# Kernel tuning notes

Measured on AMD Instinct MI355X. Metric: run time of the kernel, lower is better.

The kernel has to match this reference:

```python
import jax, jax.numpy as jnp
import numpy as np

N_NODES = 50000
N_EDGES = 800000
D_FEAT = 96
HIDDEN = 96
AVG_DEG = 16.0


def setup_inputs() -> dict:
    key = jax.random.key(0)
    k1, k2, k3, k4, k5 = jax.random.split(key, 5)
    x = jax.random.normal(k1, (N_NODES, D_FEAT), dtype=jnp.float32)
    row = jax.random.randint(k2, (N_EDGES,), 0, N_NODES)
    col = jax.random.randint(k3, (N_EDGES,), 0, N_NODES)
    edge_index = jnp.stack([row, col]).astype(jnp.int32)  # [2, E]
    # normalized adjacency values ~ 1/degree scale
    edge_weight = jax.random.uniform(k4, (N_EDGES,), dtype=jnp.float32) / AVG_DEG
    # init_w: small normal + identity (random=False path)
    W = 0.1 * jax.random.normal(k5, (D_FEAT, HIDDEN), dtype=jnp.float32) + jnp.eye(D_FEAT, HIDDEN, dtype=jnp.float32)
    b = jnp.zeros((HIDDEN,), dtype=jnp.float32)
    return {"x": x, "W": W, "b": b, "edge_index": edge_index, "edge_weight": edge_weight}


def reference(x, W, b, edge_index, edge_weight):
    # dense projection + bias
    h = x @ W + b  # [N, H]
    # sparse adj matmul: out[i] = sum_e w_e * h[col_e] for row_e == i
    row, col = edge_index[0], edge_index[1]
    msgs = edge_weight[:, None] * h[col]  # [E, H]
    pre_nonlinearity = jax.ops.segment_sum(msgs, row, num_segments=N_NODES)  # [N, H]
    # inference path: no dropout (training=None)
    output = jax.nn.elu(pre_nonlinearity)
    return (pre_nonlinearity, output)
```

## Files before the change

### kernel.cpp

```cpp
#include <hip/hip_runtime.h>


#define D 96
#define BSHIFT 5
#define BROWS 32
#define CAP 768
#define NSEGB 256
#define SCAP 16
#define NBKT_MAX 1600
#define GR 64
#define NFRAG 18

typedef unsigned long long u64;
typedef unsigned short u16;
typedef unsigned int u32;

typedef __attribute__((ext_vector_type(8))) __bf16 bf8_t;
typedef __attribute__((ext_vector_type(8))) short s8_t;
typedef __attribute__((ext_vector_type(4))) float f4_t;

__device__ __forceinline__ u16 f2bf(float f) {
  const u32 u = __float_as_uint(f);
  return (u16)((u + 0x7FFFu + ((u >> 16) & 1u)) >> 16);
}
__device__ __forceinline__ float bf2f(u16 s) {
  return __uint_as_float(((u32)s) << 16);
}

__device__ __forceinline__ f4_t mfma16(s8_t a, s8_t b, f4_t c) {
  return __builtin_amdgcn_mfma_f32_16x16x32_bf16(
      __builtin_bit_cast(bf8_t, a), __builtin_bit_cast(bf8_t, b), c, 0, 0, 0);
}

__device__ __forceinline__ void acc4(const u64* __restrict__ se, int k,
                                     const u16* __restrict__ h16, int lane,
                                     float& a0, float& a1, float& a2) {
  const u64 u0 = se[k], u1 = se[k + 1], u2 = se[k + 2], u3 = se[k + 3];
  const u16* h0 = h16 + (size_t)(u0 & 0xFFFFF) * D;
  const u16* h1 = h16 + (size_t)(u1 & 0xFFFFF) * D;
  const u16* h2 = h16 + (size_t)(u2 & 0xFFFFF) * D;
  const u16* h3 = h16 + (size_t)(u3 & 0xFFFFF) * D;
  const float w0 = __uint_as_float((u32)(u0 >> 32));
  const float w1 = __uint_as_float((u32)(u1 >> 32));
  const float w2 = __uint_as_float((u32)(u2 >> 32));
  const float w3 = __uint_as_float((u32)(u3 >> 32));
  const float p00 = bf2f(h0[lane]), p01 = bf2f(h0[lane + 32]), p02 = bf2f(h0[lane + 64]);
  const float p10 = bf2f(h1[lane]), p11 = bf2f(h1[lane + 32]), p12 = bf2f(h1[lane + 64]);
  const float p20 = bf2f(h2[lane]), p21 = bf2f(h2[lane + 32]), p22 = bf2f(h2[lane + 64]);
  const float p30 = bf2f(h3[lane]), p31 = bf2f(h3[lane + 32]), p32 = bf2f(h3[lane + 64]);
  a0 = fmaf(w0, p00, a0); a1 = fmaf(w0, p01, a1); a2 = fmaf(w0, p02, a2);
  a0 = fmaf(w1, p10, a0); a1 = fmaf(w1, p11, a1); a2 = fmaf(w1, p12, a2);
  a0 = fmaf(w2, p20, a0); a1 = fmaf(w2, p21, a1); a2 = fmaf(w2, p22, a2);
  a0 = fmaf(w3, p30, a0); a1 = fmaf(w3, p31, a1); a2 = fmaf(w3, p32, a2);
}

__device__ __forceinline__ void acc1(const u64* __restrict__ se, int k,
                                     const u16* __restrict__ h16, int lane,
                                     float& a0, float& a1, float& a2) {
  const u64 u = se[k];
  const u16* hr = h16 + (size_t)(u & 0xFFFFF) * D;
  const float w = __uint_as_float((u32)(u >> 32));
  a0 = fmaf(w, bf2f(hr[lane]), a0);
  a1 = fmaf(w, bf2f(hr[lane + 32]), a1);
  a2 = fmaf(w, bf2f(hr[lane + 64]), a2);
}

__global__ __launch_bounds__(256) void setup_kernel(
    const float* __restrict__ W, u16* __restrict__ whi, u16* __restrict__ wlo) {
  const int i = blockIdx.x * 256 + threadIdx.x;
  if (i < NFRAG * 64) {
    const int f = i >> 6;
    const int lane = i & 63;
    const int n = f / 3, kt = f - 3 * n;
    const int g = lane >> 4, l15 = lane & 15;
    const int col = n * 16 + l15;
#pragma unroll
    for (int j = 0; j < 8; ++j) {
      const float w = W[(kt * 32 + 8 * g + j) * D + col];
      const u16 hb = f2bf(w);
      whi[(size_t)(f * 64 + lane) * 8 + j] = hb;
      wlo[(size_t)(f * 64 + lane) * 8 + j] = f2bf(w - bf2f(hb));
    }
  }
}

__global__ __launch_bounds__(256) void fused_gemm_bucketize(
    const float* __restrict__ x, const u16* __restrict__ whi,
    const u16* __restrict__ wlo, const float* __restrict__ bias,
    u16* __restrict__ h16, int n_nodes,
    const int* __restrict__ rows, const int* __restrict__ cols,
    const float* __restrict__ ew, int* __restrict__ cnt_g,
    u64* __restrict__ tmp2, int n_edges, int nbkt, int echunk) {
  __shared__ int cur[NBKT_MAX];
  const int tid = threadIdx.x;

  if ((int)blockIdx.x < NSEGB) {
    const int blk = blockIdx.x;
    for (int i = tid; i < NBKT_MAX; i += 256) cur[i] = 0;
    __syncthreads();
    const int e0 = blk * echunk;
    const int e1 = min(e0 + echunk, n_edges);
    for (int e = e0 + tid; e < e1; e += 256) {
      const int r = rows[e];
      const int c = cols[e];
      const float w = ew[e];
      const int b = r >> BSHIFT;
      const u64 u = ((u64)__float_as_uint(w) << 32) |
                    ((u64)(r & (BROWS - 1)) << 20) | (u64)(unsigned)c;
      const int pos = atomicAdd(&cur[b], 1);
      if (pos < SCAP) tmp2[((size_t)b * NSEGB + blk) * SCAP + pos] = u;
    }
    __syncthreads();
    for (int b = tid; b < nbkt; b += 256)
      cnt_g[(size_t)b * NSEGB + blk] = min(cur[b], SCAP);
  } else {
    const int wid = tid >> 6;
    const int lane = tid & 63;
    const int l15 = lane & 15;
    const int g = lane >> 4;
    const int row0 = ((int)blockIdx.x - NSEGB) * GR + wid * 16;

    const int ra = min(row0 + l15, n_nodes - 1);
    const float* xr = x + (size_t)ra * D;
    s8_t ah[3], al[3];
#pragma unroll
    for (int kt = 0; kt < 3; ++kt) {
      const float4 v0 = *(const float4*)(xr + kt * 32 + 8 * g);
      const float4 v1 = *(const float4*)(xr + kt * 32 + 8 * g + 4);
      const float vv[8] = {v0.x, v0.y, v0.z, v0.w, v1.x, v1.y, v1.z, v1.w};
#pragma unroll
      for (int j = 0; j < 8; ++j) {
        const u16 hb = f2bf(vv[j]);
        ah[kt][j] = (short)hb;
        al[kt][j] = (short)f2bf(vv[j] - bf2f(hb));
      }
    }

    f4_t acc[6];
#pragma unroll
    for (int n = 0; n < 6; ++n) {
      const float bv = bias[n * 16 + l15];
      acc[n][0] = bv; acc[n][1] = bv; acc[n][2] = bv; acc[n][3] = bv;
    }

#pragma unroll
    for (int kt = 0; kt < 3; ++kt) {
#pragma unroll
      for (int n = 0; n < 6; ++n) {
        const int f = n * 3 + kt;
        const s8_t bh = *(const s8_t*)(whi + (size_t)(f * 64 + lane) * 8);
        const s8_t bl = *(const s8_t*)(wlo + (size_t)(f * 64 + lane) * 8);
        acc[n] = mfma16(ah[kt], bh, acc[n]);
        acc[n] = mfma16(al[kt], bh, acc[n]);
        acc[n] = mfma16(ah[kt], bl, acc[n]);
      }
    }

#pragma unroll
    for (int n = 0; n < 6; ++n) {
#pragma unroll
      for (int r = 0; r < 4; ++r) {
        const int row = row0 + 4 * g + r;
        if (row < n_nodes)
          h16[(size_t)row * D + n * 16 + l15] = f2bf(acc[n][r]);
      }
    }
  }
}

__global__ __launch_bounds__(256) void bucket_gather_kernel(
    const int* __restrict__ cnt_g, const u64* __restrict__ tmp2,
    const u16* __restrict__ h16, float* __restrict__ pre,
    float* __restrict__ out, int n_nodes) {
  __shared__ u64 raw[CAP];
  __shared__ u64 se[CAP];
  __shared__ int segcnt[NSEGB];
  __shared__ int segoff[NSEGB + 1];
  __shared__ int wtot[4];
  __shared__ int cnt[BROWS];
  __shared__ int off[BROWS + 1];
  __shared__ int cur[BROWS];
  const int tid = threadIdx.x;
  const int b = blockIdx.x;
  if (tid < BROWS) cnt[tid] = 0;

  const int c = min(cnt_g[(size_t)b * NSEGB + tid], SCAP);
  segcnt[tid] = c;
  int incl = c;
#pragma unroll
  for (int d = 1; d < 64; d <<= 1) {
    const int v = __shfl_up(incl, d, 64);
    if ((tid & 63) >= d) incl += v;
  }
  if ((tid & 63) == 63) wtot[tid >> 6] = incl;
  __syncthreads();
  const int w = tid >> 6;
  int wbase = 0;
#pragma unroll
  for (int ww = 0; ww < 3; ++ww)
    if (ww < w) wbase += wtot[ww];
  segoff[tid + 1] = wbase + incl;
  if (tid == 0) segoff[0] = 0;
  __syncthreads();
  int count = segoff[NSEGB];
  if (count > CAP) count = CAP;

  for (int i = tid; i < NSEGB * SCAP; i += 256) {
    const int seg = i >> 4;
    const int slot = i & 15;
    if (slot < segcnt[seg]) {
      const int p = segoff[seg] + slot;
      if (p < CAP) {
        const u64 u = tmp2[((size_t)b * NSEGB + seg) * SCAP + slot];
        raw[p] = u;
        atomicAdd(&cnt[(int)((u >> 20) & (BROWS - 1))], 1);
      }
    }
  }
  __syncthreads();

  if (tid < BROWS) {
    const int rc = cnt[tid];
    int ri = rc;
#pragma unroll
    for (int d = 1; d < BROWS; d <<= 1) {
      const int v = __shfl_up(ri, d, 64);
      if (tid >= d) ri += v;
    }
    off[tid + 1] = ri;
    if (tid == 0) off[0] = 0;
    cur[tid] = ri - rc;
  }
  __syncthreads();

  for (int k = tid; k < count; k += 256) {
    const u64 u = raw[k];
    const int rl = (int)((u >> 20) & (BROWS - 1));
    se[atomicAdd(&cur[rl], 1)] = u;
  }
  __syncthreads();

  const int g = tid >> 5;
  const int lane = tid & 31;
  const int row0 = b * BROWS;
  const int r0 = g * 4;
  int kA = off[r0 + 0]; const int eA = off[r0 + 1];
  int kB = off[r0 + 1]; const int eB = off[r0 + 2];
  int kC = off[r0 + 2]; const int eC = off[r0 + 3];
  int kD = off[r0 + 3]; const int eD = off[r0 + 4];
  float a0 = 0.f, a1 = 0.f, a2 = 0.f;
  float b0 = 0.f, b1 = 0.f, b2 = 0.f;
  float c0 = 0.f, c1 = 0.f, c2 = 0.f;
  float d0 = 0.f, d1 = 0.f, d2 = 0.f;
  while (kA + 3 < eA && kB + 3 < eB && kC + 3 < eC && kD + 3 < eD) {
    acc4(se, kA, h16, lane, a0, a1, a2);
    acc4(se, kB, h16, lane, b0, b1, b2);
    acc4(se, kC, h16, lane, c0, c1, c2);
    acc4(se, kD, h16, lane, d0, d1, d2);
    kA += 4; kB += 4; kC += 4; kD += 4;
  }
  while (kA + 3 < eA && kB + 3 < eB) {
    acc4(se, kA, h16, lane, a0, a1, a2);
    acc4(se, kB, h16, lane, b0, b1, b2);
    kA += 4; kB += 4;
  }
  while (kC + 3 < eC && kD + 3 < eD) {
    acc4(se, kC, h16, lane, c0, c1, c2);
    acc4(se, kD, h16, lane, d0, d1, d2);
    kC += 4; kD += 4;
  }
  while (kA + 3 < eA) { acc4(se, kA, h16, lane, a0, a1, a2); kA += 4; }
  while (kB + 3 < eB) { acc4(se, kB, h16, lane, b0, b1, b2); kB += 4; }
  while (kC + 3 < eC) { acc4(se, kC, h16, lane, c0, c1, c2); kC += 4; }
  while (kD + 3 < eD) { acc4(se, kD, h16, lane, d0, d1, d2); kD += 4; }
  for (; kA < eA; ++kA) acc1(se, kA, h16, lane, a0, a1, a2);
  for (; kB < eB; ++kB) acc1(se, kB, h16, lane, b0, b1, b2);
  for (; kC < eC; ++kC) acc1(se, kC, h16, lane, c0, c1, c2);
  for (; kD < eD; ++kD) acc1(se, kD, h16, lane, d0, d1, d2);

#define STORE_ROW(rr, v0, v1, v2)                                   \
  {                                                                 \
    const int row = row0 + (rr);                                    \
    if (row < n_nodes) {                                            \
      float* pr = pre + (size_t)row * D;                            \
      float* orow = out + (size_t)row * D;                          \
      pr[lane] = v0; pr[lane + 32] = v1; pr[lane + 64] = v2;        \
      orow[lane]      = v0 > 0.f ? v0 : (__expf(v0) - 1.f);         \
      orow[lane + 32] = v1 > 0.f ? v1 : (__expf(v1) - 1.f);         \
      orow[lane + 64] = v2 > 0.f ? v2 : (__expf(v2) - 1.f);         \
    }                                                               \
  }
  STORE_ROW(r0 + 0, a0, a1, a2);
  STORE_ROW(r0 + 1, b0, b1, b2);
  STORE_ROW(r0 + 2, c0, c1, c2);
  STORE_ROW(r0 + 3, d0, d1, d2);
#undef STORE_ROW
}

extern "C" void kernel_launch(void* const* d_in, const int* in_sizes, int n_in,
                              void* d_out, int out_size, void* d_ws, size_t ws_size,
                              hipStream_t stream) {
  const float* x  = (const float*)d_in[0];
  const float* W  = (const float*)d_in[1];
  const float* b  = (const float*)d_in[2];
  const int*   ei = (const int*)d_in[3];
  const float* ew = (const float*)d_in[4];

  const int n_nodes = in_sizes[0] / D;
  const int n_edges = in_sizes[4];
  const int* rows = ei;
  const int* cols = ei + n_edges;

  float* pre  = (float*)d_out;
  float* outp = pre + (size_t)n_nodes * D;

  const int nbkt = (n_nodes + BROWS - 1) / BROWS;
  const int echunk = (n_edges + NSEGB - 1) / NSEGB;

  char* ws = (char*)d_ws;
  u16*  h16   = (u16*)ws;  ws += (size_t)n_nodes * D * sizeof(u16);
  int*  cnt_g = (int*)ws;  ws += (size_t)nbkt * NSEGB * sizeof(int);
  u64*  tmp2  = (u64*)ws;  ws += (size_t)nbkt * NSEGB * SCAP * sizeof(u64);
  u16*  whi   = (u16*)ws;  ws += (size_t)NFRAG * 64 * 8 * sizeof(u16);
  u16*  wlo   = (u16*)ws;

  setup_kernel<<<(NFRAG * 64 + 255) / 256, 256, 0, stream>>>(W, whi, wlo);

  const int gb = (n_nodes + GR - 1) / GR;
  fused_gemm_bucketize<<<NSEGB + gb, 256, 0, stream>>>(
      x, whi, wlo, b, h16, n_nodes, rows, cols, ew, cnt_g, tmp2,
      n_edges, nbkt, echunk);

  bucket_gather_kernel<<<nbkt, 256, 0, stream>>>(cnt_g, tmp2, h16, pre, outp,
                                                 n_nodes);
}
```

Measured before the change: 152.6 us.

## Replace per-row edge sort with LDS float atomics in bucket gather

New measurement: 567.2 us. 3.72x slower.

```diff
diff --git a/kernel.cpp b/kernel.cpp
--- a/kernel.cpp
+++ b/kernel.cpp
@@ -30,39 +30,6 @@
 __device__ __forceinline__ f4_t mfma16(s8_t a, s8_t b, f4_t c) {
   return __builtin_amdgcn_mfma_f32_16x16x32_bf16(
       __builtin_bit_cast(bf8_t, a), __builtin_bit_cast(bf8_t, b), c, 0, 0, 0);
-}
-
-__device__ __forceinline__ void acc4(const u64* __restrict__ se, int k,
-                                     const u16* __restrict__ h16, int lane,
-                                     float& a0, float& a1, float& a2) {
-  const u64 u0 = se[k], u1 = se[k + 1], u2 = se[k + 2], u3 = se[k + 3];
-  const u16* h0 = h16 + (size_t)(u0 & 0xFFFFF) * D;
-  const u16* h1 = h16 + (size_t)(u1 & 0xFFFFF) * D;
-  const u16* h2 = h16 + (size_t)(u2 & 0xFFFFF) * D;
-  const u16* h3 = h16 + (size_t)(u3 & 0xFFFFF) * D;
-  const float w0 = __uint_as_float((u32)(u0 >> 32));
-  const float w1 = __uint_as_float((u32)(u1 >> 32));
-  const float w2 = __uint_as_float((u32)(u2 >> 32));
-  const float w3 = __uint_as_float((u32)(u3 >> 32));
-  const float p00 = bf2f(h0[lane]), p01 = bf2f(h0[lane + 32]), p02 = bf2f(h0[lane + 64]);
-  const float p10 = bf2f(h1[lane]), p11 = bf2f(h1[lane + 32]), p12 = bf2f(h1[lane + 64]);
-  const float p20 = bf2f(h2[lane]), p21 = bf2f(h2[lane + 32]), p22 = bf2f(h2[lane + 64]);
-  const float p30 = bf2f(h3[lane]), p31 = bf2f(h3[lane + 32]), p32 = bf2f(h3[lane + 64]);
-  a0 = fmaf(w0, p00, a0); a1 = fmaf(w0, p01, a1); a2 = fmaf(w0, p02, a2);
-  a0 = fmaf(w1, p10, a0); a1 = fmaf(w1, p11, a1); a2 = fmaf(w1, p12, a2);
-  a0 = fmaf(w2, p20, a0); a1 = fmaf(w2, p21, a1); a2 = fmaf(w2, p22, a2);
-  a0 = fmaf(w3, p30, a0); a1 = fmaf(w3, p31, a1); a2 = fmaf(w3, p32, a2);
-}
-
-__device__ __forceinline__ void acc1(const u64* __restrict__ se, int k,
-                                     const u16* __restrict__ h16, int lane,
-                                     float& a0, float& a1, float& a2) {
-  const u64 u = se[k];
-  const u16* hr = h16 + (size_t)(u & 0xFFFFF) * D;
-  const float w = __uint_as_float((u32)(u >> 32));
-  a0 = fmaf(w, bf2f(hr[lane]), a0);
-  a1 = fmaf(w, bf2f(hr[lane + 32]), a1);
-  a2 = fmaf(w, bf2f(hr[lane + 64]), a2);
 }
 
 __global__ __launch_bounds__(256) void setup_kernel(
@@ -173,16 +140,16 @@
     const u16* __restrict__ h16, float* __restrict__ pre,
     float* __restrict__ out, int n_nodes) {
   __shared__ u64 raw[CAP];
-  __shared__ u64 se[CAP];
+  __shared__ float accs[BROWS * D];
   __shared__ int segcnt[NSEGB];
   __shared__ int segoff[NSEGB + 1];
   __shared__ int wtot[4];
-  __shared__ int cnt[BROWS];
-  __shared__ int off[BROWS + 1];
-  __shared__ int cur[BROWS];
   const int tid = threadIdx.x;
   const int b = blockIdx.x;
-  if (tid < BROWS) cnt[tid] = 0;
+
+#pragma unroll
+  for (int i = 0; i < (BROWS * D) / 256; ++i)
+    accs[tid + i * 256] = 0.f;
 
   const int c = min(cnt_g[(size_t)b * NSEGB + tid], SCAP);
   segcnt[tid] = c;
@@ -210,91 +177,71 @@
     const int slot = i & 15;
     if (slot < segcnt[seg]) {
       const int p = segoff[seg] + slot;
-      if (p < CAP) {
-        const u64 u = tmp2[((size_t)b * NSEGB + seg) * SCAP + slot];
-        raw[p] = u;
-        atomicAdd(&cnt[(int)((u >> 20) & (BROWS - 1))], 1);
-      }
-    }
-  }
-  __syncthreads();
-
-  if (tid < BROWS) {
-    const int rc = cnt[tid];
-    int ri = rc;
-#pragma unroll
-    for (int d = 1; d < BROWS; d <<= 1) {
-      const int v = __shfl_up(ri, d, 64);
-      if (tid >= d) ri += v;
-    }
-    off[tid + 1] = ri;
-    if (tid == 0) off[0] = 0;
-    cur[tid] = ri - rc;
-  }
-  __syncthreads();
-
-  for (int k = tid; k < count; k += 256) {
-    const u64 u = raw[k];
-    const int rl = (int)((u >> 20) & (BROWS - 1));
-    se[atomicAdd(&cur[rl], 1)] = u;
+      if (p < CAP) raw[p] = tmp2[((size_t)b * NSEGB + seg) * SCAP + slot];
+    }
   }
   __syncthreads();
 
   const int g = tid >> 5;
   const int lane = tid & 31;
+  int k = g;
+  while (k + 24 < count) {
+    const u64 u0 = raw[k], u1 = raw[k + 8], u2 = raw[k + 16], u3 = raw[k + 24];
+    const u16* h0 = h16 + (size_t)(u0 & 0xFFFFF) * D;
+    const u16* h1 = h16 + (size_t)(u1 & 0xFFFFF) * D;
+    const u16* h2 = h16 + (size_t)(u2 & 0xFFFFF) * D;
+    const u16* h3 = h16 + (size_t)(u3 & 0xFFFFF) * D;
+    const float w0 = __uint_as_float((u32)(u0 >> 32));
+    const float w1 = __uint_as_float((u32)(u1 >> 32));
+    const float w2 = __uint_as_float((u32)(u2 >> 32));
+    const float w3 = __uint_as_float((u32)(u3 >> 32));
+    const int rl0 = (int)((u0 >> 20) & 31) * D;
+    const int rl1 = (int)((u1 >> 20) & 31) * D;
+    const int rl2 = (int)((u2 >> 20) & 31) * D;
+    const int rl3 = (int)((u3 >> 20) & 31) * D;
+    const float p00 = bf2f(h0[lane]), p01 = bf2f(h0[lane + 32]), p02 = bf2f(h0[lane + 64]);
+    const float p10 = bf2f(h1[lane]), p11 = bf2f(h1[lane + 32]), p12 = bf2f(h1[lane + 64]);
+    const float p20 = bf2f(h2[lane]), p21 = bf2f(h2[lane + 32]), p22 = bf2f(h2[lane + 64]);
+    const float p30 = bf2f(h3[lane]), p31 = bf2f(h3[lane + 32]), p32 = bf2f(h3[lane + 64]);
+    atomicAdd(&accs[rl0 + lane],      w0 * p00);
+    atomicAdd(&accs[rl0 + lane + 32], w0 * p01);
+    atomicAdd(&accs[rl0 + lane + 64], w0 * p02);
+    atomicAdd(&accs[rl1 + lane],      w1 * p10);
+    atomicAdd(&accs[rl1 + lane + 32], w1 * p11);
+    atomicAdd(&accs[rl1 + lane + 64], w1 * p12);
+    atomicAdd(&accs[rl2 + lane],      w2 * p20);
+    atomicAdd(&accs[rl2 + lane + 32], w2 * p21);
+    atomicAdd(&accs[rl2 + lane + 64], w2 * p22);
+    atomicAdd(&accs[rl3 + lane],      w3 * p30);
+    atomicAdd(&accs[rl3 + lane + 32], w3 * p31);
+    atomicAdd(&accs[rl3 + lane + 64], w3 * p32);
+    k += 32;
+  }
+  while (k < count) {
+    const u64 u = raw[k];
+    const u16* hr = h16 + (size_t)(u & 0xFFFFF) * D;
+    const float wv = __uint_as_float((u32)(u >> 32));
+    const int rl = (int)((u >> 20) & 31) * D;
+    atomicAdd(&accs[rl + lane],      wv * bf2f(hr[lane]));
+    atomicAdd(&accs[rl + lane + 32], wv * bf2f(hr[lane + 32]));
+    atomicAdd(&accs[rl + lane + 64], wv * bf2f(hr[lane + 64]));
+    k += 8;
+  }
+  __syncthreads();
+
   const int row0 = b * BROWS;
-  const int r0 = g * 4;
-  int kA = off[r0 + 0]; const int eA = off[r0 + 1];
-  int kB = off[r0 + 1]; const int eB = off[r0 + 2];
-  int kC = off[r0 + 2]; const int eC = off[r0 + 3];
-  int kD = off[r0 + 3]; const int eD = off[r0 + 4];
-  float a0 = 0.f, a1 = 0.f, a2 = 0.f;
-  float b0 = 0.f, b1 = 0.f, b2 = 0.f;
-  float c0 = 0.f, c1 = 0.f, c2 = 0.f;
-  float d0 = 0.f, d1 = 0.f, d2 = 0.f;
-  while (kA + 3 < eA && kB + 3 < eB && kC + 3 < eC && kD + 3 < eD) {
-    acc4(se, kA, h16, lane, a0, a1, a2);
-    acc4(se, kB, h16, lane, b0, b1, b2);
-    acc4(se, kC, h16, lane, c0, c1, c2);
-    acc4(se, kD, h16, lane, d0, d1, d2);
-    kA += 4; kB += 4; kC += 4; kD += 4;
-  }
-  while (kA + 3 < eA && kB + 3 < eB) {
-    acc4(se, kA, h16, lane, a0, a1, a2);
-    acc4(se, kB, h16, lane, b0, b1, b2);
-    kA += 4; kB += 4;
-  }
-  while (kC + 3 < eC && kD + 3 < eD) {
-    acc4(se, kC, h16, lane, c0, c1, c2);
-    acc4(se, kD, h16, lane, d0, d1, d2);
-    kC += 4; kD += 4;
-  }
-  while (kA + 3 < eA) { acc4(se, kA, h16, lane, a0, a1, a2); kA += 4; }
-  while (kB + 3 < eB) { acc4(se, kB, h16, lane, b0, b1, b2); kB += 4; }
-  while (kC + 3 < eC) { acc4(se, kC, h16, lane, c0, c1, c2); kC += 4; }
-  while (kD + 3 < eD) { acc4(se, kD, h16, lane, d0, d1, d2); kD += 4; }
-  for (; kA < eA; ++kA) acc1(se, kA, h16, lane, a0, a1, a2);
-  for (; kB < eB; ++kB) acc1(se, kB, h16, lane, b0, b1, b2);
-  for (; kC < eC; ++kC) acc1(se, kC, h16, lane, c0, c1, c2);
-  for (; kD < eD; ++kD) acc1(se, kD, h16, lane, d0, d1, d2);
-
-#define STORE_ROW(rr, v0, v1, v2)                                   \
-  {                                                                 \
-    const int row = row0 + (rr);                                    \
-    if (row < n_nodes) {                                            \
-      float* pr = pre + (size_t)row * D;                            \
-      float* orow = out + (size_t)row * D;                          \
-      pr[lane] = v0; pr[lane + 32] = v1; pr[lane + 64] = v2;        \
-      orow[lane]      = v0 > 0.f ? v0 : (__expf(v0) - 1.f);         \
-      orow[lane + 32] = v1 > 0.f ? v1 : (__expf(v1) - 1.f);         \
-      orow[lane + 64] = v2 > 0.f ? v2 : (__expf(v2) - 1.f);         \
-    }                                                               \
-  }
-  STORE_ROW(r0 + 0, a0, a1, a2);
-  STORE_ROW(r0 + 1, b0, b1, b2);
-  STORE_ROW(r0 + 2, c0, c1, c2);
-  STORE_ROW(r0 + 3, d0, d1, d2);
-#undef STORE_ROW
+  const int limit = min(BROWS * D, (n_nodes - row0) * D);
+  float* prb = pre + (size_t)row0 * D;
+  float* orb = out + (size_t)row0 * D;
+#pragma unroll
+  for (int i = 0; i < (BROWS * D) / 256; ++i) {
+    const int idx = tid + i * 256;
+    if (idx < limit) {
+      const float v = accs[idx];
+      prb[idx] = v;
+      orb[idx] = v > 0.f ? v : (__expf(v) - 1.f);
+    }
+  }
 }
 
 extern "C" void kernel_launch(void* const* d_in, const int* in_sizes, int n_in,
```
